# Kernel tuning notes

Hardware: AMD Instinct MI355X
Metric: run time of the kernel (lower is better)

The kernel has to match this reference:

```python
import jax, jax.numpy as jnp
import numpy as np

K = 3            # CRF kernel size
THETA0 = 0.5     # color bandwidth
THETA1 = 30.0    # spatial bandwidth
ALPHA0 = 3.0     # kernel scale
BASE = 0.45      # label clamping base
CRF_ITERS = 10   # mean-field iterations
NMS_SIGMA = 2.0  # gaussian matrix-NMS sigma


def _unfold(x, k=K):
    # torch.nn.Unfold(k, stride=1, padding=k//2): (B, C, H, W) -> (B, C, k*k, H*W)
    B, C, H, W = x.shape
    p = k // 2
    xp = jnp.pad(x, ((0, 0), (0, 0), (p, p), (p, p)))
    patches = jnp.stack([xp[:, :, i:i + H, j:j + W]
                         for i in range(k) for j in range(k)], axis=2)
    return patches.reshape(B, C, k * k, H * W)


def _matrix_nms(seg_masks, cate_labels, cate_scores, sigma=NMS_SIGMA):
    n = seg_masks.shape[0]
    m = seg_masks.reshape(n, -1).astype(jnp.float32)
    sum_m = m.sum(axis=1)                         # (n,)
    inter = m @ m.T                               # (n, n)
    union = sum_m[None, :] + sum_m[:, None] - inter
    triu = jnp.triu(jnp.ones((n, n), dtype=bool), k=1)
    iou = jnp.where(triu, inter / union, 0.0)
    label_eq = (cate_labels[None, :] == cate_labels[:, None]) & triu
    decay_iou = jnp.where(label_eq, iou, 0.0)
    comp = decay_iou.max(axis=0)                  # compensate IoU per candidate
    decay = jnp.exp(-sigma * decay_iou ** 2)
    compm = jnp.exp(-sigma * comp ** 2)[:, None]  # broadcast over columns (torch expand+T)
    coef = (decay / compm).min(axis=0)
    return cate_scores * coef


def _crf(feature_map, x, targets):
    B, C, H, W = feature_map.shape
    k2 = K * K
    # gaussian pairwise kernel from (shifted) color features
    fm = feature_map + 10.0
    uf = _unfold(fm)                              # (B, C, k2, H*W)
    idx = np.arange(k2)
    spatial = ((idx // K - K // 2) ** 2 + (idx % K - K // 2) ** 2).astype(np.float32)
    color = -((uf - fm.reshape(B, C, 1, H * W)) ** 2).sum(axis=1) / (2.0 * THETA0 ** 2)
    kernel = ALPHA0 * jnp.exp(color - jnp.asarray(spatial)[None, :, None] / (2.0 * THETA1 ** 2))
    kernel = kernel[:, None]                      # (B, 1, k2, H*W)

    # unary init
    xt = x * targets
    xt = (xt > 0.5).astype(jnp.float32) * (1.0 - 2.0 * BASE) + BASE
    ret = jnp.concatenate([1.0 - xt, xt], axis=1)  # (B, 2, H, W)
    ones_t = jnp.ones_like(targets)
    for _ in range(CRF_ITERS):
        uf_x = _unfold(-jnp.log(ret.reshape(2 * B, 1, H, W))).reshape(B, 2, k2, H * W)
        aggre = (uf_x * kernel).sum(axis=2)        # (B, 2, H*W)
        f = jnp.exp(-aggre).reshape(B, 2, H, W)
        f = f * jnp.concatenate([ones_t, targets], axis=1)  # gate fg channel by targets
        f = f + 1e-6
        f = f / f.sum(axis=1, keepdims=True)
        ret = (f > 0.5).astype(jnp.float32) * (1.0 - 2.0 * BASE) + BASE
    masks = (ret[:, 1:] > 0.5).astype(jnp.float32)  # (B, 1, H, W)
    count = masks.reshape(B, -1).sum(axis=1)
    valid = ((count >= H * W * 0.05) & (count <= H * W * 0.95)).astype(jnp.float32)
    return masks, valid


def setup_inputs() -> dict:
    key = jax.random.key(0)
    k1, k2, k3, k4, k5, k6 = jax.random.split(key, 6)
    n, h, w = 256, 128, 128
    ni, c = 64, 3
    seg_masks = (jax.random.uniform(k1, (n, h, w)) > 0.5).astype(jnp.float32)
    cate_scores = jnp.sort(jax.random.uniform(k2, (n,)))[::-1]
    feature_map = jax.random.uniform(k3, (ni, c, h, w))
    x = jax.random.uniform(k4, (ni, 1, h, w))
    targets = (jax.random.uniform(k5, (ni, 1, h, w)) > 0.3).astype(jnp.float32)
    cate_labels = jax.random.randint(k6, (n,), 0, 80, dtype=jnp.int64)
    return {"seg_masks": seg_masks, "cate_scores": cate_scores,
            "feature_map": feature_map, "x": x, "targets": targets,
            "cate_labels": cate_labels}


def reference(seg_masks, cate_scores, feature_map, x, targets, cate_labels):
    scores = _matrix_nms(seg_masks, cate_labels, cate_scores)
    masks, valid = _crf(feature_map, x, targets)
    return scores, masks, valid
```

## Files before the change

### kernel.cpp

```cpp
#include <hip/hip_runtime.h>
#include <stdint.h>

#define HW 16384
#define NI 64
#define NM 256
#define WORDS 256

#define PR 136
#define PSZ (26 * PR)
#define SR 34

#define OFF_STATE2 (1u << 20)
#define OFF_PACKED (2u << 20)
#define OFF_DIOUT  0x280000u
#define OFF_COMPM  0x2C0000u
#define OFF_CNT    0x2C1000u
#define OFF_GPLANE 0x300000u

__global__ __launch_bounds__(256) void diou_compm_kernel(
    const unsigned long long* __restrict__ packed, const int* __restrict__ labels,
    float* __restrict__ diouT, float* __restrict__ compm) {
    #pragma clang fp contract(off)
    __shared__ unsigned long long colj[WORDS];
    __shared__ float red[NM];
    const int j = blockIdx.x, i = threadIdx.x;
    colj[i] = packed[i * NM + j];
    __syncthreads();
    int inter = 0, si = 0, sj = 0;
    for (int w = 0; w < WORDS; ++w) {
        unsigned long long a = colj[w];
        unsigned long long b = packed[w * NM + i];
        inter += __popcll(a & b);
        sj += __popcll(a);
        si += __popcll(b);
    }
    float d = 0.0f;
    if (j > i && labels[i] == labels[j]) {
        float u = (float)(si + sj - inter);
        d = (float)inter / u;
    }
    diouT[j * NM + i] = d;
    red[i] = d;
    __syncthreads();
    for (int off = 128; off > 0; off >>= 1) {
        if (i < off) red[i] = fmaxf(red[i], red[i + off]);
        __syncthreads();
    }
    if (i == 0) {
        float m = red[0];
        float t = m * m;
        compm[j] = expf(-2.0f * t);
    }
}

template <bool FIRST>
__global__ __launch_bounds__(832, 6) void crf5_kernel(
    const float* __restrict__ feat, const float* __restrict__ scores,
    const float* __restrict__ diouT, const float* __restrict__ compm,
    const float* __restrict__ seg, unsigned long long* __restrict__ packed,
    const float* __restrict__ x, const float* __restrict__ targets,
    unsigned char* __restrict__ state2, float* __restrict__ gplane,
    float* __restrict__ out, int* __restrict__ counters) {
    #pragma clang fp contract(off)
    __shared__ float plane[4 * PSZ];
    __shared__ uint32_t stw[2][26 * SR];
    __shared__ int chg;
    const int tid = threadIdx.x, bid = blockIdx.x;
    const int img = bid >> 3, r0 = (bid & 7) * 16;
    const int w0 = r0 - 5;
    const int rel = tid >> 5;
    const int q = tid & 31;
    const int xc = q * 4;
    const int y = w0 + rel;
    const bool inimg = (unsigned)y < 128u;

    if (FIRST) {
        const int wave = tid >> 6, lane = tid & 63;
        const int gw = bid * 13 + wave;
        if (gw < 4096) {
            for (int t = 0; t < 16; ++t) {
                int gwi = gw * 16 + t;
                int i = gwi >> 8, w = gwi & 255;
                float v = seg[(size_t)i * HW + w * 64 + lane];
                unsigned long long m = __ballot(v > 0.5f);
                if (lane == 0) packed[w * NM + i] = m;
            }
        }
        if (bid == 0 && tid < NI + 1) counters[tid] = 0;
    } else {
        if (bid < NM) {
            float* red = plane;
            if (tid < NM) {
                float d = diouT[bid * NM + tid];
                float dd = d * d;
                float dec = expf(-2.0f * dd);
                red[tid] = dec / compm[tid];
            }
            __syncthreads();
            for (int off = 128; off > 0; off >>= 1) {
                if (tid < off) red[tid] = fminf(red[tid], red[tid + off]);
                __syncthreads();
            }
            if (tid == 0) out[bid] = scores[bid] * red[0];
            __syncthreads();
        }
    }

    if (FIRST) {
        const float* fb = feat + (size_t)img * 3 * HW;
        float c0[4], c1[4], c2[4];
        if (inimg) {
            const int pp = y * 128 + xc;
            float4 cv0 = *(const float4*)&fb[pp];
            float4 cv1 = *(const float4*)&fb[HW + pp];
            float4 cv2 = *(const float4*)&fb[2 * HW + pp];
            c0[0]=cv0.x+10.0f; c0[1]=cv0.y+10.0f; c0[2]=cv0.z+10.0f; c0[3]=cv0.w+10.0f;
            c1[0]=cv1.x+10.0f; c1[1]=cv1.y+10.0f; c1[2]=cv1.z+10.0f; c1[3]=cv1.w+10.0f;
            c2[0]=cv2.x+10.0f; c2[1]=cv2.y+10.0f; c2[2]=cv2.z+10.0f; c2[3]=cv2.w+10.0f;
        }
        #pragma unroll
        for (int k = 0; k < 4; ++k) {
            const int dy = (k < 3) ? -1 : 0;
            const int dx = (k < 3) ? (k - 1) : -1;
            float res[4] = {0.0f, 0.0f, 0.0f, 0.0f};
            if (inimg) {
                const int ny = y + dy;
                if ((unsigned)ny < 128u) {
                    #pragma unroll
                    for (int j = 0; j < 4; ++j) {
                        const int nx = xc + j + dx;
                        if ((unsigned)nx < 128u) {
                            const int qq = ny * 128 + nx;
                            float u0 = fb[qq] + 10.0f;
                            float u1 = fb[HW + qq] + 10.0f;
                            float u2 = fb[2 * HW + qq] + 10.0f;
                            float d0 = u0 - c0[j], d1 = u1 - c1[j], d2 = u2 - c2[j];
                            float ss = d0 * d0;
                            ss = ss + d1 * d1;
                            ss = ss + d2 * d2;
                            float color = (-ss) / 0.5f;
                            float sp = (float)(dy * dy + dx * dx) / 1800.0f;
                            res[j] = 3.0f * expf(color - sp);
                        }
                    }
                }
            }
            float4 r4 = make_float4(res[0], res[1], res[2], res[3]);
            *(float4*)&plane[k * PSZ + rel * PR + 4 + xc] = r4;
            *(float4*)&gplane[(((size_t)bid * 4 + k) * 26 + rel) * 128 + xc] = r4;
            if (q == 0)
                *(float4*)&plane[k * PSZ + rel * PR + 0] = make_float4(0, 0, 0, 0);
            if (q == 31)
                *(float4*)&plane[k * PSZ + rel * PR + 132] = make_float4(0, 0, 0, 0);
        }
    } else {
        #pragma unroll
        for (int k = 0; k < 4; ++k) {
            float4 v = *(const float4*)&gplane[(((size_t)bid * 4 + k) * 26 + rel) * 128 + xc];
            *(float4*)&plane[k * PSZ + rel * PR + 4 + xc] = v;
            if (q == 0)
                *(float4*)&plane[k * PSZ + rel * PR + 0] = make_float4(0, 0, 0, 0);
            if (q == 31)
                *(float4*)&plane[k * PSZ + rel * PR + 132] = make_float4(0, 0, 0, 0);
        }
    }
    {
        uint32_t st = 0;
        if (inimg) {
            if (FIRST) {
                const size_t gp = (size_t)img * HW + y * 128 + xc;
                const float4 xv = *(const float4*)(x + gp);
                const float4 tv = *(const float4*)(targets + gp);
                float xs[4] = {xv.x, xv.y, xv.z, xv.w};
                float ts[4] = {tv.x, tv.y, tv.z, tv.w};
                #pragma unroll
                for (int j = 0; j < 4; ++j) {
                    float xt = xs[j] * ts[j];
                    int b1 = (xt > 0.5f) ? 1 : 0;
                    int tb = (ts[j] > 0.5f) ? 1 : 0;
                    st |= (uint32_t)(b1 | ((b1 ^ 1) << 1) | (tb << 2)) << (8 * j);
                }
            } else {
                st = ((const uint32_t*)(state2 + (size_t)img * HW + y * 128))[q];
            }
        }
        stw[0][rel * SR + 1 + q] = st;
        if (!inimg) stw[1][rel * SR + 1 + q] = 0;
        if (q == 0)  { stw[0][rel * SR + 0]  = 0; stw[1][rel * SR + 0]  = 0; }
        if (q == 31) { stw[0][rel * SR + 33] = 0; stw[1][rel * SR + 33] = 0; }
    }
    __syncthreads();

    const float l45 = 0.7985076962177716f;
    const float l55 = 0.5978370007556204f;
    const bool compute = inimg && (y >= r0 - 4) && (y < r0 + 20);
    const int lane = tid & 63;
    const int rbase = rel * PR + 4 + xc;
    const int sbase = rel * SR + 1 + q;
    uint32_t pin[9];
    uint32_t powv = 0;
    bool haveprev = false;
    int cur = 0;
    for (int s = 0; s < 5; ++s) {
        if (tid == 0) chg = 0;
        __syncthreads();
        const int lo = (r0 - 4 + s < 0) ? 0 : r0 - 4 + s;
        const int hi = (r0 + 20 - s > 128) ? 128 : r0 + 20 - s;
        const bool act = compute && (y >= lo) && (y < hi);
        bool changed = false;
        if (act) {
            const uint32_t* sw = &stw[cur][0];
            uint32_t in9[9];
            #pragma unroll
            for (int r = 0; r < 3; ++r) {
                const int base = sbase + (r - 1) * SR;
                in9[r * 3 + 0] = sw[base - 1];
                in9[r * 3 + 1] = sw[base];
                in9[r * 3 + 2] = sw[base + 1];
            }
            const uint32_t wcen = in9[4];
            bool same = haveprev;
            #pragma unroll
            for (int m = 0; m < 9; ++m) same = same && (in9[m] == pin[m]);
            uint32_t ow;
            if (same) {
                ow = powv;
            } else {
                float lx1r[3][6], lx0r[3][6];
                #pragma unroll
                for (int r = 0; r < 3; ++r) {
                    const uint32_t wm = in9[r * 3 + 0];
                    const uint32_t wc = in9[r * 3 + 1];
                    const uint32_t wp = in9[r * 3 + 2];
                    unsigned char b[6];
                    b[0] = wm >> 24;
                    b[1] = wc & 0xff; b[2] = (wc >> 8) & 0xff;
                    b[3] = (wc >> 16) & 0xff; b[4] = wc >> 24;
                    b[5] = wp & 0xff;
                    #pragma unroll
                    for (int m = 0; m < 6; ++m) {
                        lx1r[r][m] = (b[m] & 1) ? l55 : l45;
                        lx0r[r][m] = (b[m] & 2) ? l55 : l45;
                    }
                }
                float4 p0a = *(const float4*)&plane[0 * PSZ + rbase];
                float4 p1a = *(const float4*)&plane[1 * PSZ + rbase];
                float4 p2a = *(const float4*)&plane[2 * PSZ + rbase];
                float4 p3a = *(const float4*)&plane[3 * PSZ + rbase];
                float4 p0b = *(const float4*)&plane[0 * PSZ + rbase + PR];
                float4 p1b = *(const float4*)&plane[1 * PSZ + rbase + PR];
                float4 p2b = *(const float4*)&plane[2 * PSZ + rbase + PR];
                float s5 = plane[3 * PSZ + rbase + 4];
                float s6 = plane[2 * PSZ + rbase + PR - 1];
                float s8 = plane[0 * PSZ + rbase + PR + 4];
                const float kw[9][4] = {
                    {p0a.x, p0a.y, p0a.z, p0a.w},
                    {p1a.x, p1a.y, p1a.z, p1a.w},
                    {p2a.x, p2a.y, p2a.z, p2a.w},
                    {p3a.x, p3a.y, p3a.z, p3a.w},
                    {3.0f, 3.0f, 3.0f, 3.0f},
                    {p3a.y, p3a.z, p3a.w, s5},
                    {s6, p2b.x, p2b.y, p2b.z},
                    {p1b.x, p1b.y, p1b.z, p1b.w},
                    {p0b.y, p0b.z, p0b.w, s8}};
                float a0[4] = {0.f, 0.f, 0.f, 0.f}, a1[4] = {0.f, 0.f, 0.f, 0.f};
                #pragma unroll
                for (int k = 0; k < 9; ++k) {
                    const int r = k / 3, m0 = k % 3;
                    #pragma unroll
                    for (int j = 0; j < 4; ++j) {
                        const float kwv = kw[k][j];
                        const float t1 = lx1r[r][j + m0] * kwv;
                        const float t0 = lx0r[r][j + m0] * kwv;
                        a1[j] = a1[j] + t1;
                        a0[j] = a0[j] + t0;
                    }
                }
                ow = 0;
                #pragma unroll
                for (int j = 0; j < 4; ++j) {
                    const unsigned char sc = (wcen >> (8 * j)) & 0xffu;
                    const float tval = (sc & 4) ? 1.0f : 0.0f;
                    const float e1 = expf(-a1[j]);
                    const float e0 = expf(-a0[j]);
                    const float m1 = e1 * tval;
                    const float f1 = m1 + 1e-6f;
                    const float f0 = e0 + 1e-6f;
                    const float den = f0 + f1;
                    const float r1 = f1 / den;
                    const float r0v = f0 / den;
                    const int s1 = (r1 > 0.5f) ? 1 : 0;
                    const int s0 = (r0v > 0.5f) ? 1 : 0;
                    ow |= (uint32_t)(s1 | (s0 << 1) | (sc & 4)) << (8 * j);
                }
                #pragma unroll
                for (int m = 0; m < 9; ++m) pin[m] = in9[m];
                powv = ow;
                haveprev = true;
            }
            stw[cur ^ 1][sbase] = ow;
            changed = (ow != wcen);
        }
        unsigned long long bal = __ballot(changed);
        if (lane == 0 && bal) atomicOr(&chg, 1);
        __syncthreads();
        if (chg == 0) break;
        cur ^= 1;
    }

    int cnt = 0;
    if (inimg && y >= r0 && y < r0 + 16) {
        const uint32_t w = stw[cur][sbase];
        if (FIRST) {
            ((uint32_t*)(state2 + (size_t)img * HW))[y * 32 + q] = w;
        } else {
            float* om = out + NM + (size_t)img * HW;
            *(float4*)(om + y * 128 + xc) =
                make_float4((float)(w & 1), (float)((w >> 8) & 1),
                            (float)((w >> 16) & 1), (float)((w >> 24) & 1));
            cnt = __popc(w & 0x01010101u);
        }
    }

    if (!FIRST) {
        __syncthreads();
        int* cred = (int*)plane;
        cred[tid] = cnt;
        if (tid < 192) cred[832 + tid] = 0;
        __syncthreads();
        for (int off = 512; off > 0; off >>= 1) {
            if (tid < off) cred[tid] += cred[tid + off];
            __syncthreads();
        }
        int* flag = (int*)&stw[0][0];
        if (tid == 0) {
            atomicAdd(&counters[img], cred[0]);
            __threadfence();
            int old = atomicAdd(&counters[NI], 1);
            flag[0] = (old == 511) ? 1 : 0;
        }
        __syncthreads();
        if (flag[0] && tid < NI) {
            int c = atomicAdd(&counters[tid], 0);
            out[NM + (size_t)NI * HW + tid] = (c >= 820 && c <= 15564) ? 1.0f : 0.0f;
        }
    }
}

extern "C" void kernel_launch(void* const* d_in, const int* in_sizes, int n_in,
                              void* d_out, int out_size, void* d_ws, size_t ws_size,
                              hipStream_t stream) {
    const float* seg = (const float*)d_in[0];
    const float* cate_scores = (const float*)d_in[1];
    const float* feat = (const float*)d_in[2];
    const float* x = (const float*)d_in[3];
    const float* targets = (const float*)d_in[4];
    const int* labels = (const int*)d_in[5];
    float* out = (float*)d_out;
    char* ws = (char*)d_ws;

    unsigned char* state2 = (unsigned char*)(ws + OFF_STATE2);
    unsigned long long* packed = (unsigned long long*)(ws + OFF_PACKED);
    float* diouT = (float*)(ws + OFF_DIOUT);
    float* compm = (float*)(ws + OFF_COMPM);
    int* counters = (int*)(ws + OFF_CNT);
    float* gplane = (float*)(ws + OFF_GPLANE);

    crf5_kernel<true><<<512, 832, 0, stream>>>(feat, cate_scores, diouT, compm,
                                               seg, packed, x, targets, state2,
                                               gplane, out, counters);
    diou_compm_kernel<<<NM, 256, 0, stream>>>(packed, labels, diouT, compm);
    crf5_kernel<false><<<512, 832, 0, stream>>>(feat, cate_scores, diouT, compm,
                                                seg, packed, x, targets, state2,
                                                gplane, out, counters);
}
```

Measured before the change: 182.5 us.

## Run all ten CRF iterations in one kernel with wider halo tiles

The CRF was previously split into two 5-iteration launches that passed state and pairwise-kernel planes through global memory. Now one kernel runs all 10 mean-field iterations. Each block covers 32 output rows plus a 10-row halo on each side, held in dynamic LDS, with each thread handling two rows. The NMS coefficient and the valid-flag finalisation move into a small third kernel, which replaces the atomic last-block pattern. The trade is more redundant halo computation (52 rows computed for 32 kept), fewer blocks (256), and higher LDS use per block in exchange for removing the global round-trip and the plane recomputation.

```diff
diff --git a/kernel.cpp b/kernel.cpp
--- a/kernel.cpp
+++ b/kernel.cpp
@@ -7,15 +7,297 @@
 #define WORDS 256
 
 #define PR 136
-#define PSZ (26 * PR)
+#define WROWS 52
+#define PSZ (WROWS * PR)
 #define SR 34
 
-#define OFF_STATE2 (1u << 20)
+#define LDS_PLANE_BYTES (4 * PSZ * 4)
+#define LDS_STW_BYTES   (2 * WROWS * SR * 4)
+#define LDS_TOTAL       (LDS_PLANE_BYTES + LDS_STW_BYTES + 16)
+
 #define OFF_PACKED (2u << 20)
 #define OFF_DIOUT  0x280000u
 #define OFF_COMPM  0x2C0000u
 #define OFF_CNT    0x2C1000u
-#define OFF_GPLANE 0x300000u
+
+__device__ __forceinline__ void build_planes_row(
+    const float* __restrict__ fb, float* __restrict__ plane, const int y,
+    const int xc, const int wrow, const int q, const bool inimg) {
+    #pragma clang fp contract(off)
+    float c0[4], c1[4], c2[4];
+    if (inimg) {
+        const int pp = y * 128 + xc;
+        float4 cv0 = *(const float4*)&fb[pp];
+        float4 cv1 = *(const float4*)&fb[HW + pp];
+        float4 cv2 = *(const float4*)&fb[2 * HW + pp];
+        c0[0]=cv0.x+10.0f; c0[1]=cv0.y+10.0f; c0[2]=cv0.z+10.0f; c0[3]=cv0.w+10.0f;
+        c1[0]=cv1.x+10.0f; c1[1]=cv1.y+10.0f; c1[2]=cv1.z+10.0f; c1[3]=cv1.w+10.0f;
+        c2[0]=cv2.x+10.0f; c2[1]=cv2.y+10.0f; c2[2]=cv2.z+10.0f; c2[3]=cv2.w+10.0f;
+    }
+    #pragma unroll
+    for (int k = 0; k < 4; ++k) {
+        const int dy = (k < 3) ? -1 : 0;
+        const int dx = (k < 3) ? (k - 1) : -1;
+        float res[4] = {0.0f, 0.0f, 0.0f, 0.0f};
+        if (inimg) {
+            const int ny = y + dy;
+            if ((unsigned)ny < 128u) {
+                #pragma unroll
+                for (int j = 0; j < 4; ++j) {
+                    const int nx = xc + j + dx;
+                    if ((unsigned)nx < 128u) {
+                        const int qq = ny * 128 + nx;
+                        float u0 = fb[qq] + 10.0f;
+                        float u1 = fb[HW + qq] + 10.0f;
+                        float u2 = fb[2 * HW + qq] + 10.0f;
+                        float d0 = u0 - c0[j], d1 = u1 - c1[j], d2 = u2 - c2[j];
+                        float ss = d0 * d0;
+                        ss = ss + d1 * d1;
+                        ss = ss + d2 * d2;
+                        float color = (-ss) / 0.5f;
+                        float sp = (float)(dy * dy + dx * dx) / 1800.0f;
+                        res[j] = 3.0f * expf(color - sp);
+                    }
+                }
+            }
+        }
+        *(float4*)&plane[k * PSZ + wrow * PR + 4 + xc] =
+            make_float4(res[0], res[1], res[2], res[3]);
+        if (q == 0)
+            *(float4*)&plane[k * PSZ + wrow * PR + 0] = make_float4(0, 0, 0, 0);
+        if (q == 31)
+            *(float4*)&plane[k * PSZ + wrow * PR + 132] = make_float4(0, 0, 0, 0);
+    }
+}
+
+__device__ __forceinline__ void stage_init_row(
+    const float* __restrict__ x, const float* __restrict__ targets,
+    uint32_t* __restrict__ stw0, uint32_t* __restrict__ stw1, const int img,
+    const int y, const int wrow, const int q, const int xc, const bool inimg) {
+    #pragma clang fp contract(off)
+    uint32_t st = 0;
+    if (inimg) {
+        const size_t gp = (size_t)img * HW + y * 128 + xc;
+        const float4 xv = *(const float4*)(x + gp);
+        const float4 tv = *(const float4*)(targets + gp);
+        float xs[4] = {xv.x, xv.y, xv.z, xv.w};
+        float ts[4] = {tv.x, tv.y, tv.z, tv.w};
+        #pragma unroll
+        for (int j = 0; j < 4; ++j) {
+            float xt = xs[j] * ts[j];
+            int b1 = (xt > 0.5f) ? 1 : 0;
+            int tb = (ts[j] > 0.5f) ? 1 : 0;
+            st |= (uint32_t)(b1 | ((b1 ^ 1) << 1) | (tb << 2)) << (8 * j);
+        }
+    }
+    stw0[wrow * SR + 1 + q] = st;
+    if (!inimg) stw1[wrow * SR + 1 + q] = 0;
+    if (q == 0)  { stw0[wrow * SR + 0]  = 0; stw1[wrow * SR + 0]  = 0; }
+    if (q == 31) { stw0[wrow * SR + 33] = 0; stw1[wrow * SR + 33] = 0; }
+}
+
+__device__ __forceinline__ uint32_t crf_cell(
+    const float* __restrict__ plane, const uint32_t* __restrict__ sw,
+    const int rbase, const int sbase, uint32_t (&pin)[9], uint32_t& powv,
+    bool& haveprev, uint32_t& wcen_out) {
+    #pragma clang fp contract(off)
+    const float l45 = 0.7985076962177716f;
+    const float l55 = 0.5978370007556204f;
+    uint32_t in9[9];
+    #pragma unroll
+    for (int r = 0; r < 3; ++r) {
+        const int base = sbase + (r - 1) * SR;
+        in9[r * 3 + 0] = sw[base - 1];
+        in9[r * 3 + 1] = sw[base];
+        in9[r * 3 + 2] = sw[base + 1];
+    }
+    const uint32_t wcen = in9[4];
+    wcen_out = wcen;
+    bool same = haveprev;
+    #pragma unroll
+    for (int m = 0; m < 9; ++m) same = same && (in9[m] == pin[m]);
+    if (same) return powv;
+
+    float lx1r[3][6], lx0r[3][6];
+    #pragma unroll
+    for (int r = 0; r < 3; ++r) {
+        const uint32_t wm = in9[r * 3 + 0];
+        const uint32_t wc = in9[r * 3 + 1];
+        const uint32_t wp = in9[r * 3 + 2];
+        unsigned char b[6];
+        b[0] = wm >> 24;
+        b[1] = wc & 0xff; b[2] = (wc >> 8) & 0xff;
+        b[3] = (wc >> 16) & 0xff; b[4] = wc >> 24;
+        b[5] = wp & 0xff;
+        #pragma unroll
+        for (int m = 0; m < 6; ++m) {
+            lx1r[r][m] = (b[m] & 1) ? l55 : l45;
+            lx0r[r][m] = (b[m] & 2) ? l55 : l45;
+        }
+    }
+    float4 p0a = *(const float4*)&plane[0 * PSZ + rbase];
+    float4 p1a = *(const float4*)&plane[1 * PSZ + rbase];
+    float4 p2a = *(const float4*)&plane[2 * PSZ + rbase];
+    float4 p3a = *(const float4*)&plane[3 * PSZ + rbase];
+    float4 p0b = *(const float4*)&plane[0 * PSZ + rbase + PR];
+    float4 p1b = *(const float4*)&plane[1 * PSZ + rbase + PR];
+    float4 p2b = *(const float4*)&plane[2 * PSZ + rbase + PR];
+    float s5 = plane[3 * PSZ + rbase + 4];
+    float s6 = plane[2 * PSZ + rbase + PR - 1];
+    float s8 = plane[0 * PSZ + rbase + PR + 4];
+    const float kw[9][4] = {
+        {p0a.x, p0a.y, p0a.z, p0a.w},
+        {p1a.x, p1a.y, p1a.z, p1a.w},
+        {p2a.x, p2a.y, p2a.z, p2a.w},
+        {p3a.x, p3a.y, p3a.z, p3a.w},
+        {3.0f, 3.0f, 3.0f, 3.0f},
+        {p3a.y, p3a.z, p3a.w, s5},
+        {s6, p2b.x, p2b.y, p2b.z},
+        {p1b.x, p1b.y, p1b.z, p1b.w},
+        {p0b.y, p0b.z, p0b.w, s8}};
+    float a0[4] = {0.f, 0.f, 0.f, 0.f}, a1[4] = {0.f, 0.f, 0.f, 0.f};
+    #pragma unroll
+    for (int k = 0; k < 9; ++k) {
+        const int r = k / 3, m0 = k % 3;
+        #pragma unroll
+        for (int j = 0; j < 4; ++j) {
+            const float kwv = kw[k][j];
+            const float t1 = lx1r[r][j + m0] * kwv;
+            const float t0 = lx0r[r][j + m0] * kwv;
+            a1[j] = a1[j] + t1;
+            a0[j] = a0[j] + t0;
+        }
+    }
+    uint32_t ow = 0;
+    #pragma unroll
+    for (int j = 0; j < 4; ++j) {
+        const unsigned char sc = (wcen >> (8 * j)) & 0xffu;
+        const float tval = (sc & 4) ? 1.0f : 0.0f;
+        const float e1 = expf(-a1[j]);
+        const float e0 = expf(-a0[j]);
+        const float m1 = e1 * tval;
+        const float f1 = m1 + 1e-6f;
+        const float f0 = e0 + 1e-6f;
+        const float den = f0 + f1;
+        const float r1 = f1 / den;
+        const float r0v = f0 / den;
+        const int s1 = (r1 > 0.5f) ? 1 : 0;
+        const int s0 = (r0v > 0.5f) ? 1 : 0;
+        ow |= (uint32_t)(s1 | (s0 << 1) | (sc & 4)) << (8 * j);
+    }
+    #pragma unroll
+    for (int m = 0; m < 9; ++m) pin[m] = in9[m];
+    powv = ow;
+    haveprev = true;
+    return ow;
+}
+
+__global__ __launch_bounds__(832, 4) void crf10_kernel(
+    const float* __restrict__ feat, const float* __restrict__ seg,
+    unsigned long long* __restrict__ packed, const float* __restrict__ x,
+    const float* __restrict__ targets, float* __restrict__ out,
+    int* __restrict__ counters) {
+    #pragma clang fp contract(off)
+    extern __shared__ char smem[];
+    float* plane = (float*)smem;
+    uint32_t* stw0 = (uint32_t*)(smem + LDS_PLANE_BYTES);
+    uint32_t* stw1 = stw0 + WROWS * SR;
+    int* chg = (int*)(smem + LDS_PLANE_BYTES + LDS_STW_BYTES);
+    uint32_t* const stwb[2] = {stw0, stw1};
+
+    const int tid = threadIdx.x, bid = blockIdx.x;
+    const int img = bid >> 2;
+    const int r0 = (bid & 3) * 32;
+    const int relp = tid >> 5;
+    const int q = tid & 31;
+    const int xc = q * 4;
+    const int wrowA = 2 * relp, wrowB = 2 * relp + 1;
+    const int yA = r0 - 10 + wrowA, yB = yA + 1;
+    const bool inA = (unsigned)yA < 128u, inB = (unsigned)yB < 128u;
+    const int rbaseA = wrowA * PR + 4 + xc, rbaseB = wrowB * PR + 4 + xc;
+    const int sbaseA = wrowA * SR + 1 + q,  sbaseB = wrowB * SR + 1 + q;
+    const float* fb = feat + (size_t)img * 3 * HW;
+
+    {
+        const int wave = tid >> 6, lane = tid & 63;
+        const int gw = bid * 13 + wave;
+        for (int gwi = gw; gwi < 65536; gwi += 3328) {
+            const int i = gwi >> 8, w = gwi & 255;
+            float v = seg[(size_t)i * HW + w * 64 + lane];
+            unsigned long long m = __ballot(v > 0.5f);
+            if (lane == 0) packed[w * NM + i] = m;
+        }
+    }
+
+    build_planes_row(fb, plane, yA, xc, wrowA, q, inA);
+    build_planes_row(fb, plane, yB, xc, wrowB, q, inB);
+    stage_init_row(x, targets, stw0, stw1, img, yA, wrowA, q, xc, inA);
+    stage_init_row(x, targets, stw0, stw1, img, yB, wrowB, q, xc, inB);
+    __syncthreads();
+
+    uint32_t pinA[9], pinB[9];
+    uint32_t powvA = 0, powvB = 0;
+    bool hpA = false, hpB = false;
+    int cur = 0;
+    for (int s = 0; s < 10; ++s) {
+        if (tid == 0) *chg = 0;
+        __syncthreads();
+        const int lo = (r0 - 9 + s < 0) ? 0 : r0 - 9 + s;
+        const int hi = (r0 + 41 - s > 128) ? 128 : r0 + 41 - s;
+        const uint32_t* sw = stwb[cur];
+        uint32_t* swn = stwb[cur ^ 1];
+        bool changed = false;
+        if (yA >= lo && yA < hi) {
+            uint32_t wcen;
+            uint32_t ow = crf_cell(plane, sw, rbaseA, sbaseA, pinA, powvA, hpA, wcen);
+            swn[sbaseA] = ow;
+            changed = (ow != wcen);
+        }
+        if (yB >= lo && yB < hi) {
+            uint32_t wcen;
+            uint32_t ow = crf_cell(plane, sw, rbaseB, sbaseB, pinB, powvB, hpB, wcen);
+            swn[sbaseB] = ow;
+            changed = changed || (ow != wcen);
+        }
+        unsigned long long bal = __ballot(changed);
+        if ((tid & 63) == 0 && bal) atomicOr(chg, 1);
+        __syncthreads();
+        if (*chg == 0) break;
+        cur ^= 1;
+    }
+
+    int cnt = 0;
+    {
+        const uint32_t* swf = stwb[cur];
+        float* om = out + NM + (size_t)img * HW;
+        if (yA >= r0 && yA < r0 + 32) {
+            const uint32_t w = swf[sbaseA];
+            *(float4*)(om + yA * 128 + xc) =
+                make_float4((float)(w & 1), (float)((w >> 8) & 1),
+                            (float)((w >> 16) & 1), (float)((w >> 24) & 1));
+            cnt += __popc(w & 0x01010101u);
+        }
+        if (yB >= r0 && yB < r0 + 32) {
+            const uint32_t w = swf[sbaseB];
+            *(float4*)(om + yB * 128 + xc) =
+                make_float4((float)(w & 1), (float)((w >> 8) & 1),
+                            (float)((w >> 16) & 1), (float)((w >> 24) & 1));
+            cnt += __popc(w & 0x01010101u);
+        }
+    }
+    __syncthreads();
+    {
+        int* cred = (int*)plane;
+        cred[tid] = cnt;
+        if (tid < 192) cred[832 + tid] = 0;
+        __syncthreads();
+        for (int off = 512; off > 0; off >>= 1) {
+            if (tid < off) cred[tid] += cred[tid + off];
+            __syncthreads();
+        }
+        if (tid == 0) counters[bid] = cred[0];
+    }
+}
 
 __global__ __launch_bounds__(256) void diou_compm_kernel(
     const unsigned long long* __restrict__ packed, const int* __restrict__ labels,
@@ -53,297 +335,27 @@
     }
 }
 
-template <bool FIRST>
-__global__ __launch_bounds__(832, 6) void crf5_kernel(
-    const float* __restrict__ feat, const float* __restrict__ scores,
-    const float* __restrict__ diouT, const float* __restrict__ compm,
-    const float* __restrict__ seg, unsigned long long* __restrict__ packed,
-    const float* __restrict__ x, const float* __restrict__ targets,
-    unsigned char* __restrict__ state2, float* __restrict__ gplane,
-    float* __restrict__ out, int* __restrict__ counters) {
-    #pragma clang fp contract(off)
-    __shared__ float plane[4 * PSZ];
-    __shared__ uint32_t stw[2][26 * SR];
-    __shared__ int chg;
-    const int tid = threadIdx.x, bid = blockIdx.x;
-    const int img = bid >> 3, r0 = (bid & 7) * 16;
-    const int w0 = r0 - 5;
-    const int rel = tid >> 5;
-    const int q = tid & 31;
-    const int xc = q * 4;
-    const int y = w0 + rel;
-    const bool inimg = (unsigned)y < 128u;
-
-    if (FIRST) {
-        const int wave = tid >> 6, lane = tid & 63;
-        const int gw = bid * 13 + wave;
-        if (gw < 4096) {
-            for (int t = 0; t < 16; ++t) {
-                int gwi = gw * 16 + t;
-                int i = gwi >> 8, w = gwi & 255;
-                float v = seg[(size_t)i * HW + w * 64 + lane];
-                unsigned long long m = __ballot(v > 0.5f);
-                if (lane == 0) packed[w * NM + i] = m;
-            }
-        }
-        if (bid == 0 && tid < NI + 1) counters[tid] = 0;
-    } else {
-        if (bid < NM) {
-            float* red = plane;
-            if (tid < NM) {
-                float d = diouT[bid * NM + tid];
-                float dd = d * d;
-                float dec = expf(-2.0f * dd);
-                red[tid] = dec / compm[tid];
-            }
-            __syncthreads();
-            for (int off = 128; off > 0; off >>= 1) {
-                if (tid < off) red[tid] = fminf(red[tid], red[tid + off]);
-                __syncthreads();
-            }
-            if (tid == 0) out[bid] = scores[bid] * red[0];
-            __syncthreads();
-        }
-    }
-
-    if (FIRST) {
-        const float* fb = feat + (size_t)img * 3 * HW;
-        float c0[4], c1[4], c2[4];
-        if (inimg) {
-            const int pp = y * 128 + xc;
-            float4 cv0 = *(const float4*)&fb[pp];
-            float4 cv1 = *(const float4*)&fb[HW + pp];
-            float4 cv2 = *(const float4*)&fb[2 * HW + pp];
-            c0[0]=cv0.x+10.0f; c0[1]=cv0.y+10.0f; c0[2]=cv0.z+10.0f; c0[3]=cv0.w+10.0f;
-            c1[0]=cv1.x+10.0f; c1[1]=cv1.y+10.0f; c1[2]=cv1.z+10.0f; c1[3]=cv1.w+10.0f;
-            c2[0]=cv2.x+10.0f; c2[1]=cv2.y+10.0f; c2[2]=cv2.z+10.0f; c2[3]=cv2.w+10.0f;
-        }
-        #pragma unroll
-        for (int k = 0; k < 4; ++k) {
-            const int dy = (k < 3) ? -1 : 0;
-            const int dx = (k < 3) ? (k - 1) : -1;
-            float res[4] = {0.0f, 0.0f, 0.0f, 0.0f};
-            if (inimg) {
-                const int ny = y + dy;
-                if ((unsigned)ny < 128u) {
-                    #pragma unroll
-                    for (int j = 0; j < 4; ++j) {
-                        const int nx = xc + j + dx;
-                        if ((unsigned)nx < 128u) {
-                            const int qq = ny * 128 + nx;
-                            float u0 = fb[qq] + 10.0f;
-                            float u1 = fb[HW + qq] + 10.0f;
-                            float u2 = fb[2 * HW + qq] + 10.0f;
-                            float d0 = u0 - c0[j], d1 = u1 - c1[j], d2 = u2 - c2[j];
-                            float ss = d0 * d0;
-                            ss = ss + d1 * d1;
-                            ss = ss + d2 * d2;
-                            float color = (-ss) / 0.5f;
-                            float sp = (float)(dy * dy + dx * dx) / 1800.0f;
-                            res[j] = 3.0f * expf(color - sp);
-                        }
-                    }
-                }
-            }
-            float4 r4 = make_float4(res[0], res[1], res[2], res[3]);
-            *(float4*)&plane[k * PSZ + rel * PR + 4 + xc] = r4;
-            *(float4*)&gplane[(((size_t)bid * 4 + k) * 26 + rel) * 128 + xc] = r4;
-            if (q == 0)
-                *(float4*)&plane[k * PSZ + rel * PR + 0] = make_float4(0, 0, 0, 0);
-            if (q == 31)
-                *(float4*)&plane[k * PSZ + rel * PR + 132] = make_float4(0, 0, 0, 0);
-        }
-    } else {
-        #pragma unroll
-        for (int k = 0; k < 4; ++k) {
-            float4 v = *(const float4*)&gplane[(((size_t)bid * 4 + k) * 26 + rel) * 128 + xc];
-            *(float4*)&plane[k * PSZ + rel * PR + 4 + xc] = v;
-            if (q == 0)
-                *(float4*)&plane[k * PSZ + rel * PR + 0] = make_float4(0, 0, 0, 0);
-            if (q == 31)
-                *(float4*)&plane[k * PSZ + rel * PR + 132] = make_float4(0, 0, 0, 0);
-        }
-    }
-    {
-        uint32_t st = 0;
-        if (inimg) {
-            if (FIRST) {
-                const size_t gp = (size_t)img * HW + y * 128 + xc;
-                const float4 xv = *(const float4*)(x + gp);
-                const float4 tv = *(const float4*)(targets + gp);
-                float xs[4] = {xv.x, xv.y, xv.z, xv.w};
-                float ts[4] = {tv.x, tv.y, tv.z, tv.w};
-                #pragma unroll
-                for (int j = 0; j < 4; ++j) {
-                    float xt = xs[j] * ts[j];
-                    int b1 = (xt > 0.5f) ? 1 : 0;
-                    int tb = (ts[j] > 0.5f) ? 1 : 0;
-                    st |= (uint32_t)(b1 | ((b1 ^ 1) << 1) | (tb << 2)) << (8 * j);
-                }
-            } else {
-                st = ((const uint32_t*)(state2 + (size_t)img * HW + y * 128))[q];
-            }
-        }
-        stw[0][rel * SR + 1 + q] = st;
-        if (!inimg) stw[1][rel * SR + 1 + q] = 0;
-        if (q == 0)  { stw[0][rel * SR + 0]  = 0; stw[1][rel * SR + 0]  = 0; }
-        if (q == 31) { stw[0][rel * SR + 33] = 0; stw[1][rel * SR + 33] = 0; }
-    }
-    __syncthreads();
-
-    const float l45 = 0.7985076962177716f;
-    const float l55 = 0.5978370007556204f;
-    const bool compute = inimg && (y >= r0 - 4) && (y < r0 + 20);
-    const int lane = tid & 63;
-    const int rbase = rel * PR + 4 + xc;
-    const int sbase = rel * SR + 1 + q;
-    uint32_t pin[9];
-    uint32_t powv = 0;
-    bool haveprev = false;
-    int cur = 0;
-    for (int s = 0; s < 5; ++s) {
-        if (tid == 0) chg = 0;
-        __syncthreads();
-        const int lo = (r0 - 4 + s < 0) ? 0 : r0 - 4 + s;
-        const int hi = (r0 + 20 - s > 128) ? 128 : r0 + 20 - s;
-        const bool act = compute && (y >= lo) && (y < hi);
-        bool changed = false;
-        if (act) {
-            const uint32_t* sw = &stw[cur][0];
-            uint32_t in9[9];
-            #pragma unroll
-            for (int r = 0; r < 3; ++r) {
-                const int base = sbase + (r - 1) * SR;
-                in9[r * 3 + 0] = sw[base - 1];
-                in9[r * 3 + 1] = sw[base];
-                in9[r * 3 + 2] = sw[base + 1];
-            }
-            const uint32_t wcen = in9[4];
-            bool same = haveprev;
-            #pragma unroll
-            for (int m = 0; m < 9; ++m) same = same && (in9[m] == pin[m]);
-            uint32_t ow;
-            if (same) {
-                ow = powv;
-            } else {
-                float lx1r[3][6], lx0r[3][6];
-                #pragma unroll
-                for (int r = 0; r < 3; ++r) {
-                    const uint32_t wm = in9[r * 3 + 0];
-                    const uint32_t wc = in9[r * 3 + 1];
-                    const uint32_t wp = in9[r * 3 + 2];
-                    unsigned char b[6];
-                    b[0] = wm >> 24;
-                    b[1] = wc & 0xff; b[2] = (wc >> 8) & 0xff;
-                    b[3] = (wc >> 16) & 0xff; b[4] = wc >> 24;
-                    b[5] = wp & 0xff;
-                    #pragma unroll
-                    for (int m = 0; m < 6; ++m) {
-                        lx1r[r][m] = (b[m] & 1) ? l55 : l45;
-                        lx0r[r][m] = (b[m] & 2) ? l55 : l45;
-                    }
-                }
-                float4 p0a = *(const float4*)&plane[0 * PSZ + rbase];
-                float4 p1a = *(const float4*)&plane[1 * PSZ + rbase];
-                float4 p2a = *(const float4*)&plane[2 * PSZ + rbase];
-                float4 p3a = *(const float4*)&plane[3 * PSZ + rbase];
-                float4 p0b = *(const float4*)&plane[0 * PSZ + rbase + PR];
-                float4 p1b = *(const float4*)&plane[1 * PSZ + rbase + PR];
-                float4 p2b = *(const float4*)&plane[2 * PSZ + rbase + PR];
-                float s5 = plane[3 * PSZ + rbase + 4];
-                float s6 = plane[2 * PSZ + rbase + PR - 1];
-                float s8 = plane[0 * PSZ + rbase + PR + 4];
-                const float kw[9][4] = {
-                    {p0a.x, p0a.y, p0a.z, p0a.w},
-                    {p1a.x, p1a.y, p1a.z, p1a.w},
-                    {p2a.x, p2a.y, p2a.z, p2a.w},
-                    {p3a.x, p3a.y, p3a.z, p3a.w},
-                    {3.0f, 3.0f, 3.0f, 3.0f},
-                    {p3a.y, p3a.z, p3a.w, s5},
-                    {s6, p2b.x, p2b.y, p2b.z},
-                    {p1b.x, p1b.y, p1b.z, p1b.w},
-                    {p0b.y, p0b.z, p0b.w, s8}};
-                float a0[4] = {0.f, 0.f, 0.f, 0.f}, a1[4] = {0.f, 0.f, 0.f, 0.f};
-                #pragma unroll
-                for (int k = 0; k < 9; ++k) {
-                    const int r = k / 3, m0 = k % 3;
-                    #pragma unroll
-                    for (int j = 0; j < 4; ++j) {
-                        const float kwv = kw[k][j];
-                        const float t1 = lx1r[r][j + m0] * kwv;
-                        const float t0 = lx0r[r][j + m0] * kwv;
-                        a1[j] = a1[j] + t1;
-                        a0[j] = a0[j] + t0;
-                    }
-                }
-                ow = 0;
-                #pragma unroll
-                for (int j = 0; j < 4; ++j) {
-                    const unsigned char sc = (wcen >> (8 * j)) & 0xffu;
-                    const float tval = (sc & 4) ? 1.0f : 0.0f;
-                    const float e1 = expf(-a1[j]);
-                    const float e0 = expf(-a0[j]);
-                    const float m1 = e1 * tval;
-                    const float f1 = m1 + 1e-6f;
-                    const float f0 = e0 + 1e-6f;
-                    const float den = f0 + f1;
-                    const float r1 = f1 / den;
-                    const float r0v = f0 / den;
-                    const int s1 = (r1 > 0.5f) ? 1 : 0;
-                    const int s0 = (r0v > 0.5f) ? 1 : 0;
-                    ow |= (uint32_t)(s1 | (s0 << 1) | (sc & 4)) << (8 * j);
-                }
-                #pragma unroll
-                for (int m = 0; m < 9; ++m) pin[m] = in9[m];
-                powv = ow;
-                haveprev = true;
-            }
-            stw[cur ^ 1][sbase] = ow;
-            changed = (ow != wcen);
-        }
-        unsigned long long bal = __ballot(changed);
-        if (lane == 0 && bal) atomicOr(&chg, 1);
-        __syncthreads();
-        if (chg == 0) break;
-        cur ^= 1;
-    }
-
-    int cnt = 0;
-    if (inimg && y >= r0 && y < r0 + 16) {
-        const uint32_t w = stw[cur][sbase];
-        if (FIRST) {
-            ((uint32_t*)(state2 + (size_t)img * HW))[y * 32 + q] = w;
-        } else {
-            float* om = out + NM + (size_t)img * HW;
-            *(float4*)(om + y * 128 + xc) =
-                make_float4((float)(w & 1), (float)((w >> 8) & 1),
-                            (float)((w >> 16) & 1), (float)((w >> 24) & 1));
-            cnt = __popc(w & 0x01010101u);
-        }
-    }
-
-    if (!FIRST) {
-        __syncthreads();
-        int* cred = (int*)plane;
-        cred[tid] = cnt;
-        if (tid < 192) cred[832 + tid] = 0;
-        __syncthreads();
-        for (int off = 512; off > 0; off >>= 1) {
-            if (tid < off) cred[tid] += cred[tid + off];
-            __syncthreads();
-        }
-        int* flag = (int*)&stw[0][0];
-        if (tid == 0) {
-            atomicAdd(&counters[img], cred[0]);
-            __threadfence();
-            int old = atomicAdd(&counters[NI], 1);
-            flag[0] = (old == 511) ? 1 : 0;
-        }
-        __syncthreads();
-        if (flag[0] && tid < NI) {
-            int c = atomicAdd(&counters[tid], 0);
-            out[NM + (size_t)NI * HW + tid] = (c >= 820 && c <= 15564) ? 1.0f : 0.0f;
-        }
+__global__ __launch_bounds__(256) void coef_valid_kernel(
+    const float* __restrict__ scores, const float* __restrict__ diouT,
+    const float* __restrict__ compm, const int* __restrict__ counters,
+    float* __restrict__ out) {
+    #pragma clang fp contract(off)
+    __shared__ float red[NM];
+    const int bid = blockIdx.x, tid = threadIdx.x;
+    float d = diouT[bid * NM + tid];
+    float dd = d * d;
+    float dec = expf(-2.0f * dd);
+    red[tid] = dec / compm[tid];
+    __syncthreads();
+    for (int off = 128; off > 0; off >>= 1) {
+        if (tid < off) red[tid] = fminf(red[tid], red[tid + off]);
+        __syncthreads();
+    }
+    if (tid == 0) out[bid] = scores[bid] * red[0];
+    if (bid == 0 && tid < NI) {
+        int c = counters[4 * tid] + counters[4 * tid + 1] +
+                counters[4 * tid + 2] + counters[4 * tid + 3];
+        out[NM + (size_t)NI * HW + tid] = (c >= 820 && c <= 15564) ? 1.0f : 0.0f;
     }
 }
 
@@ -359,18 +371,22 @@
     float* out = (float*)d_out;
     char* ws = (char*)d_ws;
 
-    unsigned char* state2 = (unsigned char*)(ws + OFF_STATE2);
     unsigned long long* packed = (unsigned long long*)(ws + OFF_PACKED);
     float* diouT = (float*)(ws + OFF_DIOUT);
     float* compm = (float*)(ws + OFF_COMPM);
     int* counters = (int*)(ws + OFF_CNT);
-    float* gplane = (float*)(ws + OFF_GPLANE);
-
-    crf5_kernel<true><<<512, 832, 0, stream>>>(feat, cate_scores, diouT, compm,
-                                               seg, packed, x, targets, state2,
-                                               gplane, out, counters);
+
+    static bool attr_done = false;
+    if (!attr_done) {
+        (void)hipFuncSetAttribute((const void*)crf10_kernel,
+                                  hipFuncAttributeMaxDynamicSharedMemorySize,
+                                  LDS_TOTAL);
+        attr_done = true;
+    }
+
+    crf10_kernel<<<256, 832, LDS_TOTAL, stream>>>(feat, seg, packed, x, targets,
+                                                  out, counters);
     diou_compm_kernel<<<NM, 256, 0, stream>>>(packed, labels, diouT, compm);
-    crf5_kernel<false><<<512, 832, 0, stream>>>(feat, cate_scores, diouT, compm,
-                                                seg, packed, x, targets, state2,
-                                                gplane, out, counters);
-}
+    coef_valid_kernel<<<NM, 256, 0, stream>>>(cate_scores, diouT, compm,
+                                              counters, out);
+}
```

After: 170.4 us. -6.6%, faster.
